# Kernel tuning notes

Hardware: AMD Instinct MI355X
Metric: run time of the kernel (lower is better)

## Reference

```python
import jax, jax.numpy as jnp
import numpy as np
from jax import lax


def _gru_layer(x, w_ih, w_hh, b_ih, b_hh):
    """PyTorch-style GRU layer (gate order r, z, n). x: [B,T,I] -> ([B,T,H], [B,H])."""
    B, T, _ = x.shape
    H = w_hh.shape[1]
    # Precompute all input-side gate projections in one big GEMM: [B,T,3H]
    xg = jnp.einsum('bti,gi->btg', x, w_ih) + b_ih

    def step(h, xg_t):
        hg = h @ w_hh.T + b_hh                      # [B,3H]
        xr, xz, xn = jnp.split(xg_t, 3, axis=-1)
        hr, hz, hn = jnp.split(hg, 3, axis=-1)
        r = jax.nn.sigmoid(xr + hr)
        z = jax.nn.sigmoid(xz + hz)
        n = jnp.tanh(xn + r * hn)
        h_new = (1.0 - z) * n + z * h
        return h_new, h_new

    h0 = jnp.zeros((B, H), dtype=x.dtype)
    h_last, hs = lax.scan(step, h0, jnp.swapaxes(xg, 0, 1))  # scan over time
    return jnp.swapaxes(hs, 0, 1), h_last


def setup_inputs() -> dict:
    key = jax.random.key(0)
    ks = jax.random.split(key, 13)
    B, T, I, H = 64, 512, 2048, 128

    def u(k, shape, fan_in):
        bound = 1.0 / np.sqrt(fan_in)
        return jax.random.uniform(k, shape, jnp.float32, -bound, bound)

    return {
        'x': jax.random.normal(ks[0], (B, T, I), jnp.float32),
        'w_ih0': u(ks[1], (3 * H, I), H),
        'w_hh0': u(ks[2], (3 * H, H), H),
        'b_ih0': u(ks[3], (3 * H,), H),
        'b_hh0': u(ks[4], (3 * H,), H),
        'w_ih1': u(ks[5], (3 * H, H), H),
        'w_hh1': u(ks[6], (3 * H, H), H),
        'b_ih1': u(ks[7], (3 * H,), H),
        'b_hh1': u(ks[8], (3 * H,), H),
        'w_fc1': u(ks[9], (64, H), H),
        'b_fc1': u(ks[10], (64,), H),
        'w_fc2': u(ks[11], (1, 64), 64),
        'b_fc2': u(ks[12], (1,), 64),
    }


def reference(x, w_ih0, w_hh0, b_ih0, b_hh0, w_ih1, w_hh1, b_ih1, b_hh1,
              w_fc1, b_fc1, w_fc2, b_fc2):
    # 2-layer GRU (inter-layer dropout is identity in eval mode)
    h1_seq, _ = _gru_layer(x, w_ih0, w_hh0, b_ih0, b_hh0)
    _, h_last = _gru_layer(h1_seq, w_ih1, w_hh1, b_ih1, b_hh1)
    # MLP head: fc1 -> ReLU -> (dropout=identity in eval) -> fc2
    y = jax.nn.relu(h_last @ w_fc1.T + b_fc1)
    return y @ w_fc2.T + b_fc2  # [B, 1]
```

## Files before the change

### kernel.cpp

```cpp
#include <hip/hip_runtime.h>
#include <cstdint>
#include <cstddef>

typedef float f32x4 __attribute__((ext_vector_type(4)));
typedef float f32x2 __attribute__((ext_vector_type(2)));
typedef short s16x8 __attribute__((ext_vector_type(8)));
typedef unsigned short u16;

static __device__ __forceinline__ u16 f2bf(float f) {
    uint32_t x = __float_as_uint(f);
    x += 0x7fffu + ((x >> 16) & 1u);
    return (u16)(x >> 16);
}
static __device__ __forceinline__ float bf2f(u16 h) {
    return __uint_as_float(((uint32_t)h) << 16);
}

static __device__ __forceinline__ void bar_lds() {
    asm volatile("s_waitcnt lgkmcnt(0)" ::: "memory");
    __builtin_amdgcn_s_barrier();
    asm volatile("" ::: "memory");
}

__global__ void k_zero(int* __restrict__ p, int n) {
    int i = blockIdx.x * 256 + threadIdx.x;
    if (i < n) p[i] = 0;
}

__global__ void k_split(const float* __restrict__ src, u16* __restrict__ hi,
                        u16* __restrict__ lo, int n) {
    int i = blockIdx.x * 256 + threadIdx.x;
    if (i < n) {
        float f = src[i];
        u16 h = f2bf(f);
        hi[i] = h;
        lo[i] = f2bf(f - bf2f(h));
    }
}

__global__ __launch_bounds__(256, 2)
void k_gemm(const float* __restrict__ A, const u16* __restrict__ Wh,
            const u16* __restrict__ Wl, const float* __restrict__ bias,
            float* __restrict__ C, int K) {
    __shared__ __align__(16) u16 sm[32768];

    const int tid  = threadIdx.x;
    const int lane = tid & 63;
    const int wave = tid >> 6;
    const int wm = wave >> 1, wn = wave & 1;

    int g = blockIdx.x;
    int xcd = g & 7, ix = g >> 3;
    int q3 = ix / 3;
    int mb = xcd + 8 * q3;
    int nb = ix - 3 * q3;
    const long m0 = (long)mb * 128;
    const int  n0 = nb * 128;

    f32x4 acc[4][4];
    const f32x4 vzero = {0.f, 0.f, 0.f, 0.f};
#pragma unroll
    for (int i = 0; i < 4; ++i)
#pragma unroll
        for (int j = 0; j < 4; ++j) acc[i][j] = vzero;

    const int ar = tid >> 1;
    const int ac = (tid & 1) * 16;
    const float* aptr = A + (m0 + ar) * (long)K + ac;
    const int br = tid >> 2;
    const int bc = (tid & 3) * 8;
    const u16* bhp = Wh + (long)(n0 + br) * K + bc;
    const u16* blp = Wl + (long)(n0 + br) * K + bc;

    const int ksteps = K >> 5;
    f32x4 a0, a1, a2, a3;

    {
        a0 = *(const f32x4*)(aptr + 0);
        a1 = *(const f32x4*)(aptr + 4);
        a2 = *(const f32x4*)(aptr + 8);
        a3 = *(const f32x4*)(aptr + 12);
#pragma unroll
        for (int c = 0; c < 2; ++c) {
            const u16* sh = bhp + (long)(c * 64) * K;
            const u16* sl = blp + (long)(c * 64) * K;
            u16* dh = &sm[8192  + c * 2048 + wave * 512];
            u16* dl = &sm[12288 + c * 2048 + wave * 512];
            __builtin_amdgcn_global_load_lds((const __attribute__((address_space(1))) void*)sh,
                                             (__attribute__((address_space(3))) void*)dh, 16, 0, 0);
            __builtin_amdgcn_global_load_lds((const __attribute__((address_space(1))) void*)sl,
                                             (__attribute__((address_space(3))) void*)dl, 16, 0, 0);
        }
        float fr[16] = {a0.x,a0.y,a0.z,a0.w, a1.x,a1.y,a1.z,a1.w,
                        a2.x,a2.y,a2.z,a2.w, a3.x,a3.y,a3.z,a3.w};
        s16x8 h0, h1, l0, l1;
#pragma unroll
        for (int i = 0; i < 8; ++i) {
            u16 hh = f2bf(fr[i]);     h0[i] = (short)hh; l0[i] = (short)f2bf(fr[i] - bf2f(hh));
            u16 hh2 = f2bf(fr[8+i]);  h1[i] = (short)hh2; l1[i] = (short)f2bf(fr[8+i] - bf2f(hh2));
        }
        u16* dh = &sm[ar * 32 + ac];
        u16* dl = &sm[4096 + ar * 32 + ac];
        *(s16x8*)dh = h0; *(s16x8*)(dh + 8) = h1;
        *(s16x8*)dl = l0; *(s16x8*)(dl + 8) = l1;
    }
    __syncthreads();

    for (int ks = 0; ks < ksteps; ++ks) {
        const int cur = ks & 1, nxt = cur ^ 1;
        const bool more = (ks + 1 < ksteps);
        if (more) {
            const int k0 = (ks + 1) << 5;
            a0 = *(const f32x4*)(aptr + k0 + 0);
            a1 = *(const f32x4*)(aptr + k0 + 4);
            a2 = *(const f32x4*)(aptr + k0 + 8);
            a3 = *(const f32x4*)(aptr + k0 + 12);
#pragma unroll
            for (int c = 0; c < 2; ++c) {
                const u16* sh = bhp + (long)(c * 64) * K + k0;
                const u16* sl = blp + (long)(c * 64) * K + k0;
                u16* dh = &sm[nxt * 16384 + 8192  + c * 2048 + wave * 512];
                u16* dl = &sm[nxt * 16384 + 12288 + c * 2048 + wave * 512];
                __builtin_amdgcn_global_load_lds((const __attribute__((address_space(1))) void*)sh,
                                                 (__attribute__((address_space(3))) void*)dh, 16, 0, 0);
                __builtin_amdgcn_global_load_lds((const __attribute__((address_space(1))) void*)sl,
                                                 (__attribute__((address_space(3))) void*)dl, 16, 0, 0);
            }
        }
        {
            const u16* base = &sm[cur * 16384];
            const int koff = (lane >> 4) * 8;
            const int rsel = lane & 15;
            s16x8 ah[4], al[4];
#pragma unroll
            for (int f = 0; f < 4; ++f) {
                int row = wm * 64 + f * 16 + rsel;
                ah[f] = *(const s16x8*)&base[row * 32 + koff];
                al[f] = *(const s16x8*)&base[4096 + row * 32 + koff];
            }
#pragma unroll
            for (int j = 0; j < 4; ++j) {
                int row = wn * 64 + j * 16 + rsel;
                s16x8 bh = *(const s16x8*)&base[8192  + row * 32 + koff];
                s16x8 bl = *(const s16x8*)&base[12288 + row * 32 + koff];
#pragma unroll
                for (int f = 0; f < 4; ++f) {
                    acc[f][j] = __builtin_amdgcn_mfma_f32_16x16x32_bf16(ah[f], bh, acc[f][j], 0, 0, 0);
                    acc[f][j] = __builtin_amdgcn_mfma_f32_16x16x32_bf16(ah[f], bl, acc[f][j], 0, 0, 0);
                    acc[f][j] = __builtin_amdgcn_mfma_f32_16x16x32_bf16(al[f], bh, acc[f][j], 0, 0, 0);
                }
            }
        }
        if (more) {
            float fr[16] = {a0.x,a0.y,a0.z,a0.w, a1.x,a1.y,a1.z,a1.w,
                            a2.x,a2.y,a2.z,a2.w, a3.x,a3.y,a3.z,a3.w};
            s16x8 h0, h1, l0, l1;
#pragma unroll
            for (int i = 0; i < 8; ++i) {
                u16 hh = f2bf(fr[i]);     h0[i] = (short)hh; l0[i] = (short)f2bf(fr[i] - bf2f(hh));
                u16 hh2 = f2bf(fr[8+i]);  h1[i] = (short)hh2; l1[i] = (short)f2bf(fr[8+i] - bf2f(hh2));
            }
            u16* dh = &sm[nxt * 16384 + ar * 32 + ac];
            u16* dl = &sm[nxt * 16384 + 4096 + ar * 32 + ac];
            *(s16x8*)dh = h0; *(s16x8*)(dh + 8) = h1;
            *(s16x8*)dl = l0; *(s16x8*)(dl + 8) = l1;
        }
        __syncthreads();
    }

    const int r0 = (lane >> 4) << 2;
    const int cn = lane & 15;
#pragma unroll
    for (int f = 0; f < 4; ++f) {
        const long mrow = m0 + wm * 64 + f * 16 + r0;
#pragma unroll
        for (int j = 0; j < 4; ++j) {
            const int n = n0 + wn * 64 + j * 16 + cn;
            const float bv = bias[n];
            float* o = C + mrow * 384 + n;
#pragma unroll
            for (int jj = 0; jj < 4; ++jj) o[(long)jj * 384] = acc[f][j][jj] + bv;
        }
    }
}


struct SmemRecur { float hsh[128]; float hp[8][384]; };
struct SmemGemm  { u16 ah[16 * 128]; u16 al[16 * 128]; };
union Smem {
    SmemRecur r;
    SmemGemm  g;
    char force_one_block_per_cu[98304];
};

#define R_ISSUE(BUF, G) do {                                                  \
    const int _G = (G);                                                       \
    if (_G < 128 && tid < 128) {                                              \
        if (!isL0 && (_G & 3) == 0) {                                         \
            if ((tid & 63) == 0) {                                            \
                while (atomicAdd(&waitflag[b * 32 + (_G >> 2)], 0) == 0)      \
                    __builtin_amdgcn_s_sleep(8);                              \
            }                                                                 \
            __threadfence();                                                  \
        }                                                                     \
        const float* _p = xgb + (size_t)(4 * _G) * 384 + tid;                 \
        BUF[0] = _p[0];    BUF[1] = _p[128];   BUF[2]  = _p[256];             \
        BUF[3] = _p[384];  BUF[4] = _p[512];   BUF[5]  = _p[640];             \
        BUF[6] = _p[768];  BUF[7] = _p[896];   BUF[8]  = _p[1024];            \
        BUF[9] = _p[1152]; BUF[10] = _p[1280]; BUF[11] = _p[1408];            \
    } } while (0)

#define R_STEP(T, BUF, J) do {                                                \
    const int _t = (T);                                                       \
    f32x4 _h0 = *(const f32x4*)(sm.hsh + 16 * w + 0);                         \
    f32x4 _h1 = *(const f32x4*)(sm.hsh + 16 * w + 4);                         \
    f32x4 _h2 = *(const f32x4*)(sm.hsh + 16 * w + 8);                         \
    f32x4 _h3 = *(const f32x4*)(sm.hsh + 16 * w + 12);                        \
    float _ha[16];                                                            \
    _ha[0]=_h0[0];  _ha[1]=_h0[1];  _ha[2]=_h0[2];  _ha[3]=_h0[3];            \
    _ha[4]=_h1[0];  _ha[5]=_h1[1];  _ha[6]=_h1[2];  _ha[7]=_h1[3];            \
    _ha[8]=_h2[0];  _ha[9]=_h2[1];  _ha[10]=_h2[2]; _ha[11]=_h2[3];           \
    _ha[12]=_h3[0]; _ha[13]=_h3[1]; _ha[14]=_h3[2]; _ha[15]=_h3[3];           \
    float _s0=0.f,_s1=0.f,_s2=0.f,_s3=0.f,_s4=0.f,_s5=0.f;                    \
    _Pragma("unroll")                                                         \
    for (int _i = 0; _i < 16; ++_i) {                                         \
        const float _hv = _ha[_i];                                            \
        _s0 = fmaf(_hv, wr[0][_i], _s0); _s1 = fmaf(_hv, wr[1][_i], _s1);     \
        _s2 = fmaf(_hv, wr[2][_i], _s2); _s3 = fmaf(_hv, wr[3][_i], _s3);     \
        _s4 = fmaf(_hv, wr[4][_i], _s4); _s5 = fmaf(_hv, wr[5][_i], _s5);     \
    }                                                                         \
    *(f32x2*)&sm.hp[w][g6 + 0] = (f32x2){_s0, _s1};                           \
    *(f32x2*)&sm.hp[w][g6 + 2] = (f32x2){_s2, _s3};                           \
    *(f32x2*)&sm.hp[w][g6 + 4] = (f32x2){_s4, _s5};                           \
    const bool _pub = isL0 && _t > 0 && (_t & 15) == 0;                       \
    if (_pub && tid < 128) asm volatile("s_waitcnt vmcnt(12)" ::: "memory");  \
    bar_lds();                                                                \
    if (_pub && tid == 0) {                                                   \
        __threadfence();                                                      \
        atomicExch(&setflag[b * 32 + ((_t >> 4) - 1)], 1);                    \
    }                                                                         \
    if (tid < 128) {                                                          \
        const int _c = tid;                                                   \
        float _hr = bhr, _hz = bhz, _hn = bhn;                                \
        _Pragma("unroll")                                                     \
        for (int _q = 0; _q < 8; ++_q) {                                      \
            _hr += sm.hp[_q][_c];                                             \
            _hz += sm.hp[_q][128 + _c];                                       \
            _hn += sm.hp[_q][256 + _c];                                       \
        }                                                                     \
        const float _xr = BUF[(J) * 3 + 0];                                   \
        const float _xz = BUF[(J) * 3 + 1];                                   \
        const float _xn = BUF[(J) * 3 + 2];                                   \
        const float _r = 1.f / (1.f + __expf(-(_xr + _hr)));                  \
        const float _z = 1.f / (1.f + __expf(-(_xz + _hz)));                  \
        float _a = _xn + _r * _hn;                                            \
        _a = fminf(fmaxf(_a, -15.f), 15.f);                                   \
        const float _e = __expf(2.f * _a);                                    \
        const float _n = (_e - 1.f) / (_e + 1.f);                             \
        hreg = (1.f - _z) * _n + _z * hreg;                                   \
        sm.hsh[_c] = hreg;                                                    \
        if (isL0) hseq[((size_t)(b * 512 + _t)) * 128 + _c] = hreg;           \
    }                                                                         \
    bar_lds();                                                                \
} while (0)

__device__ __forceinline__ void recur_role(
    bool isL0, int b, const float* __restrict__ xg,
    const float* __restrict__ whh, const float* __restrict__ bhh,
    float* __restrict__ hseq, int* __restrict__ setflag, int* __restrict__ waitflag,
    const float* __restrict__ wfc1, const float* __restrict__ bfc1,
    const float* __restrict__ wfc2, const float* __restrict__ bfc2,
    float* __restrict__ out, SmemRecur& sm)
{
    const int tid  = threadIdx.x;
    const int w    = tid >> 6;
    const int lane = tid & 63;
    const int g6   = 6 * lane;

    float wr[6][16];
#pragma unroll
    for (int j = 0; j < 6; ++j) {
        const float* p = whh + (size_t)(g6 + j) * 128 + 16 * w;
#pragma unroll
        for (int i4 = 0; i4 < 4; ++i4) {
            f32x4 v = *(const f32x4*)(p + 4 * i4);
            wr[j][4*i4+0] = v[0]; wr[j][4*i4+1] = v[1];
            wr[j][4*i4+2] = v[2]; wr[j][4*i4+3] = v[3];
        }
    }
    float bhr = 0.f, bhz = 0.f, bhn = 0.f, hreg = 0.f;
    if (tid < 128) {
        bhr = bhh[tid]; bhz = bhh[128 + tid]; bhn = bhh[256 + tid];
        sm.hsh[tid] = 0.f;
    }
    const float* xgb = xg + (size_t)b * 512 * 384;

    float pA[12], pB[12];
    R_ISSUE(pA, 0);
    R_ISSUE(pB, 1);
    __syncthreads();

    for (int gp = 0; gp < 64; ++gp) {
        const int t0 = gp * 8;
        R_STEP(t0 + 0, pA, 0); R_STEP(t0 + 1, pA, 1);
        R_STEP(t0 + 2, pA, 2); R_STEP(t0 + 3, pA, 3);
        R_ISSUE(pA, 2 * gp + 2);
        R_STEP(t0 + 4, pB, 0); R_STEP(t0 + 5, pB, 1);
        R_STEP(t0 + 6, pB, 2); R_STEP(t0 + 7, pB, 3);
        R_ISSUE(pB, 2 * gp + 3);
    }

    if (isL0) {
        if (tid < 128) asm volatile("s_waitcnt vmcnt(0)" ::: "memory");
        __syncthreads();
        if (tid == 0) { __threadfence(); atomicExch(&setflag[b * 32 + 31], 1); }
    }

    if (!isL0 && tid < 64) {
        const float* wv = wfc1 + tid * 128;
        float acc = bfc1[tid];
#pragma unroll 8
        for (int c = 0; c < 128; ++c) acc = fmaf(sm.hsh[c], wv[c], acc);
        float p = fmaxf(acc, 0.f) * wfc2[tid];
#pragma unroll
        for (int off = 32; off > 0; off >>= 1) p += __shfl_down(p, off);
        if (tid == 0) out[b] = p + bfc2[0];
    }
}

__device__ __forceinline__ void worker_role(
    int wk, const float* __restrict__ h1, float* __restrict__ xg,
    const float* __restrict__ wih1, const float* __restrict__ bih1,
    int* __restrict__ h1flag, int* __restrict__ xgflag, SmemGemm& sm)
{
    const int tid = threadIdx.x, lane = tid & 63, w = tid >> 6;
    const int rsel = lane & 15, koff = (lane >> 4) * 8;

    s16x8 bh[3][4], bl[3][4];
    float bias[3];
#pragma unroll
    for (int nfi = 0; nfi < 3; ++nfi) {
        const int n = (3 * w + nfi) * 16 + rsel;
        bias[nfi] = bih1[n];
#pragma unroll
        for (int ks = 0; ks < 4; ++ks) {
            const float* p = wih1 + n * 128 + ks * 32 + koff;
            f32x4 v0 = *(const f32x4*)p, v1 = *(const f32x4*)(p + 4);
            float fv[8] = {v0[0],v0[1],v0[2],v0[3], v1[0],v1[1],v1[2],v1[3]};
            s16x8 hh, ll;
#pragma unroll
            for (int i = 0; i < 8; ++i) {
                u16 h = f2bf(fv[i]); hh[i] = (short)h; ll[i] = (short)f2bf(fv[i] - bf2f(h));
            }
            bh[nfi][ks] = hh; bl[nfi][ks] = ll;
        }
    }

    for (int j = wk; j < 2048; j += 128) {
        const int c = j >> 6, b = j & 63;
        if (tid == 0) {
            while (atomicAdd(&h1flag[b * 32 + c], 0) == 0) __builtin_amdgcn_s_sleep(8);
            __threadfence();
        }
        __syncthreads();
        if (tid < 256) {
            const int r = tid >> 4, c0 = (tid & 15) * 8;
            const float* p = h1 + ((size_t)(b * 512 + c * 16 + r)) * 128 + c0;
            f32x4 v0 = *(const f32x4*)p, v1 = *(const f32x4*)(p + 4);
            float fv[8] = {v0[0],v0[1],v0[2],v0[3], v1[0],v1[1],v1[2],v1[3]};
            s16x8 hh, ll;
#pragma unroll
            for (int i = 0; i < 8; ++i) {
                u16 h = f2bf(fv[i]); hh[i] = (short)h; ll[i] = (short)f2bf(fv[i] - bf2f(h));
            }
            const int sc = c0 ^ ((r & 7) << 3);
            *(s16x8*)&sm.ah[r * 128 + sc] = hh;
            *(s16x8*)&sm.al[r * 128 + sc] = ll;
        }
        __syncthreads();

        f32x4 acc[3];
        const f32x4 vz = {0.f, 0.f, 0.f, 0.f};
        acc[0] = vz; acc[1] = vz; acc[2] = vz;
#pragma unroll
        for (int ks = 0; ks < 4; ++ks) {
            const int si = rsel * 128 + ((ks * 32 + koff) ^ ((rsel & 7) << 3));
            s16x8 a_h = *(const s16x8*)&sm.ah[si];
            s16x8 a_l = *(const s16x8*)&sm.al[si];
#pragma unroll
            for (int nfi = 0; nfi < 3; ++nfi) {
                acc[nfi] = __builtin_amdgcn_mfma_f32_16x16x32_bf16(a_h, bh[nfi][ks], acc[nfi], 0, 0, 0);
                acc[nfi] = __builtin_amdgcn_mfma_f32_16x16x32_bf16(a_h, bl[nfi][ks], acc[nfi], 0, 0, 0);
                acc[nfi] = __builtin_amdgcn_mfma_f32_16x16x32_bf16(a_l, bh[nfi][ks], acc[nfi], 0, 0, 0);
            }
        }
#pragma unroll
        for (int nfi = 0; nfi < 3; ++nfi) {
            const int n = (3 * w + nfi) * 16 + rsel;
#pragma unroll
            for (int jj = 0; jj < 4; ++jj) {
                const int m = (lane >> 4) * 4 + jj;
                xg[((size_t)(b * 512 + c * 16 + m)) * 384 + n] = acc[nfi][jj] + bias[nfi];
            }
        }
        __syncthreads();
        if (tid == 0) {
            __threadfence();
            atomicExch(&xgflag[b * 32 + c], 1);
        }
    }
}

__global__ __launch_bounds__(512, 2)
void k_fused(float* __restrict__ xg, float* __restrict__ h1,
             const float* __restrict__ whh0, const float* __restrict__ bhh0,
             const float* __restrict__ wih1, const float* __restrict__ bih1,
             const float* __restrict__ whh1, const float* __restrict__ bhh1,
             const float* __restrict__ wfc1, const float* __restrict__ bfc1,
             const float* __restrict__ wfc2, const float* __restrict__ bfc2,
             float* __restrict__ out, int* __restrict__ h1flag, int* __restrict__ xgflag)
{
    __shared__ __align__(16) Smem sm;
    const int bid = blockIdx.x;
    if (bid < 64) {
        recur_role(true, bid, xg, whh0, bhh0, h1, h1flag, nullptr,
                   nullptr, nullptr, nullptr, nullptr, nullptr, sm.r);
    } else if (bid < 128) {
        recur_role(false, bid - 64, xg, whh1, bhh1, nullptr, nullptr, xgflag,
                   wfc1, bfc1, wfc2, bfc2, out, sm.r);
    } else {
        worker_role(bid - 128, h1, xg, wih1, bih1, h1flag, xgflag, sm.g);
    }
}

extern "C" void kernel_launch(void* const* d_in, const int* in_sizes, int n_in,
                              void* d_out, int out_size, void* d_ws, size_t ws_size,
                              hipStream_t stream) {
    const float* x     = (const float*)d_in[0];
    const float* w_ih0 = (const float*)d_in[1];
    const float* w_hh0 = (const float*)d_in[2];
    const float* b_ih0 = (const float*)d_in[3];
    const float* b_hh0 = (const float*)d_in[4];
    const float* w_ih1 = (const float*)d_in[5];
    const float* w_hh1 = (const float*)d_in[6];
    const float* b_ih1 = (const float*)d_in[7];
    const float* b_hh1 = (const float*)d_in[8];
    const float* w_fc1 = (const float*)d_in[9];
    const float* b_fc1 = (const float*)d_in[10];
    const float* w_fc2 = (const float*)d_in[11];
    const float* b_fc2 = (const float*)d_in[12];
    float* out = (float*)d_out;
    (void)in_sizes; (void)n_in; (void)out_size; (void)ws_size;

    char* ws = (char*)d_ws;
    float* xg     = (float*)(ws + 0);
    float* h1     = (float*)(ws + 50331648);
    u16*   w0h    = (u16*)(ws + 67108864);
    u16*   w0l    = (u16*)(ws + 68681728);
    int*   h1flag = (int*)(ws + 70254592);
    int*   xgflag = h1flag + 2048;

    k_zero<<<16, 256, 0, stream>>>(h1flag, 4096);
    k_split<<<3072, 256, 0, stream>>>(w_ih0, w0h, w0l, 384 * 2048);
    k_gemm<<<768, 256, 0, stream>>>(x, w0h, w0l, b_ih0, xg, 2048);
    k_fused<<<256, 512, 0, stream>>>(xg, h1, w_hh0, b_hh0, w_ih1, b_ih1,
                                     w_hh1, b_hh1, w_fc1, b_fc1, w_fc2, b_fc2,
                                     out, h1flag, xgflag);
}
```

Measured before the change: 621.9 us.

## Batch 16 sequences per recurrent block using split-bf16 MFMA for hidden GEMM

Each recurrent block now handles 16 batch rows instead of one, so only 8 blocks run the GRU recurrences. The h @ W_hh product moves from scalar FMAs with an LDS partial-sum reduction to 3-term split-bf16 MFMA, with h double-buffered as bf16 hi/lo fragments in LDS, which removes one barrier per step. Worker blocks grow to 248, signal with per-group counters, and the launch bound is relaxed to one block per CU. The aim is to shorten the serial per-timestep critical path, at the cost of split-bf16 precision error and coarser synchronisation.

```diff
diff --git a/kernel.cpp b/kernel.cpp
--- a/kernel.cpp
+++ b/kernel.cpp
@@ -3,7 +3,6 @@
 #include <cstddef>
 
 typedef float f32x4 __attribute__((ext_vector_type(4)));
-typedef float f32x2 __attribute__((ext_vector_type(2)));
 typedef short s16x8 __attribute__((ext_vector_type(8)));
 typedef unsigned short u16;
 
@@ -185,153 +184,176 @@
 }
 
 
-struct SmemRecur { float hsh[128]; float hp[8][384]; };
-struct SmemGemm  { u16 ah[16 * 128]; u16 al[16 * 128]; };
+struct SmemRecur {
+    u16 frag[2][2][2048];
+    float h2buf[16][128];
+};
+struct SmemGemm  { u16 ah[2048]; u16 al[2048]; };
 union Smem {
     SmemRecur r;
     SmemGemm  g;
     char force_one_block_per_cu[98304];
 };
 
-#define R_ISSUE(BUF, G) do {                                                  \
-    const int _G = (G);                                                       \
-    if (_G < 128 && tid < 128) {                                              \
-        if (!isL0 && (_G & 3) == 0) {                                         \
-            if ((tid & 63) == 0) {                                            \
-                while (atomicAdd(&waitflag[b * 32 + (_G >> 2)], 0) == 0)      \
+#define PF(R_, Z_, N_, T_) do {                                               \
+    const int _pt = (T_);                                                     \
+    if (_pt < 512) {                                                          \
+        if (!isL0 && (_pt & 15) == 0) {                                       \
+            if (lane == 0) {                                                  \
+                while (atomicAdd(&waitcnt[g * 32 + (_pt >> 4)], 0) < 16)      \
                     __builtin_amdgcn_s_sleep(8);                              \
             }                                                                 \
             __threadfence();                                                  \
         }                                                                     \
-        const float* _p = xgb + (size_t)(4 * _G) * 384 + tid;                 \
-        BUF[0] = _p[0];    BUF[1] = _p[128];   BUF[2]  = _p[256];             \
-        BUF[3] = _p[384];  BUF[4] = _p[512];   BUF[5]  = _p[640];             \
-        BUF[6] = _p[768];  BUF[7] = _p[896];   BUF[8]  = _p[1024];            \
-        BUF[9] = _p[1152]; BUF[10] = _p[1280]; BUF[11] = _p[1408];            \
+        const size_t _o = (size_t)_pt * 384;                                  \
+        R_[0] = bp0[_o]; Z_[0] = bp0[_o + 128]; N_[0] = bp0[_o + 256];        \
+        R_[1] = bp1[_o]; Z_[1] = bp1[_o + 128]; N_[1] = bp1[_o + 256];        \
+        R_[2] = bp2[_o]; Z_[2] = bp2[_o + 128]; N_[2] = bp2[_o + 256];        \
+        R_[3] = bp3[_o]; Z_[3] = bp3[_o + 128]; N_[3] = bp3[_o + 256];        \
     } } while (0)
 
-#define R_STEP(T, BUF, J) do {                                                \
-    const int _t = (T);                                                       \
-    f32x4 _h0 = *(const f32x4*)(sm.hsh + 16 * w + 0);                         \
-    f32x4 _h1 = *(const f32x4*)(sm.hsh + 16 * w + 4);                         \
-    f32x4 _h2 = *(const f32x4*)(sm.hsh + 16 * w + 8);                         \
-    f32x4 _h3 = *(const f32x4*)(sm.hsh + 16 * w + 12);                        \
-    float _ha[16];                                                            \
-    _ha[0]=_h0[0];  _ha[1]=_h0[1];  _ha[2]=_h0[2];  _ha[3]=_h0[3];            \
-    _ha[4]=_h1[0];  _ha[5]=_h1[1];  _ha[6]=_h1[2];  _ha[7]=_h1[3];            \
-    _ha[8]=_h2[0];  _ha[9]=_h2[1];  _ha[10]=_h2[2]; _ha[11]=_h2[3];           \
-    _ha[12]=_h3[0]; _ha[13]=_h3[1]; _ha[14]=_h3[2]; _ha[15]=_h3[3];           \
-    float _s0=0.f,_s1=0.f,_s2=0.f,_s3=0.f,_s4=0.f,_s5=0.f;                    \
-    _Pragma("unroll")                                                         \
-    for (int _i = 0; _i < 16; ++_i) {                                         \
-        const float _hv = _ha[_i];                                            \
-        _s0 = fmaf(_hv, wr[0][_i], _s0); _s1 = fmaf(_hv, wr[1][_i], _s1);     \
-        _s2 = fmaf(_hv, wr[2][_i], _s2); _s3 = fmaf(_hv, wr[3][_i], _s3);     \
-        _s4 = fmaf(_hv, wr[4][_i], _s4); _s5 = fmaf(_hv, wr[5][_i], _s5);     \
+#define RSTEP(T_, R_, Z_, N_) do {                                            \
+    const int _t = (T_);                                                      \
+    f32x4 accr = {R_[0] + bhr, R_[1] + bhr, R_[2] + bhr, R_[3] + bhr};        \
+    f32x4 accz = {Z_[0] + bhz, Z_[1] + bhz, Z_[2] + bhz, Z_[3] + bhz};        \
+    f32x4 accn = {bhn, bhn, bhn, bhn};                                        \
+    const float _xn0 = N_[0], _xn1 = N_[1], _xn2 = N_[2], _xn3 = N_[3];       \
+    {                                                                         \
+        const u16* _hb = &sm.frag[p][0][0];                                   \
+        const u16* _lb = &sm.frag[p][1][0];                                   \
+        _Pragma("unroll")                                                     \
+        for (int kk = 0; kk < 4; ++kk) {                                      \
+            const int _fo = (kk * 4 + qk) * 128 + col * 8;                    \
+            s16x8 _ah = *(const s16x8*)&_hb[_fo];                             \
+            s16x8 _al = *(const s16x8*)&_lb[_fo];                             \
+            accr = __builtin_amdgcn_mfma_f32_16x16x32_bf16(_ah, wbh[0][kk], accr, 0, 0, 0); \
+            accz = __builtin_amdgcn_mfma_f32_16x16x32_bf16(_ah, wbh[1][kk], accz, 0, 0, 0); \
+            accn = __builtin_amdgcn_mfma_f32_16x16x32_bf16(_ah, wbh[2][kk], accn, 0, 0, 0); \
+            accr = __builtin_amdgcn_mfma_f32_16x16x32_bf16(_ah, wbl[0][kk], accr, 0, 0, 0); \
+            accz = __builtin_amdgcn_mfma_f32_16x16x32_bf16(_ah, wbl[1][kk], accz, 0, 0, 0); \
+            accn = __builtin_amdgcn_mfma_f32_16x16x32_bf16(_ah, wbl[2][kk], accn, 0, 0, 0); \
+            accr = __builtin_amdgcn_mfma_f32_16x16x32_bf16(_al, wbh[0][kk], accr, 0, 0, 0); \
+            accz = __builtin_amdgcn_mfma_f32_16x16x32_bf16(_al, wbh[1][kk], accz, 0, 0, 0); \
+            accn = __builtin_amdgcn_mfma_f32_16x16x32_bf16(_al, wbh[2][kk], accn, 0, 0, 0); \
+        }                                                                     \
     }                                                                         \
-    *(f32x2*)&sm.hp[w][g6 + 0] = (f32x2){_s0, _s1};                           \
-    *(f32x2*)&sm.hp[w][g6 + 2] = (f32x2){_s2, _s3};                           \
-    *(f32x2*)&sm.hp[w][g6 + 4] = (f32x2){_s4, _s5};                           \
-    const bool _pub = isL0 && _t > 0 && (_t & 15) == 0;                       \
-    if (_pub && tid < 128) asm volatile("s_waitcnt vmcnt(12)" ::: "memory");  \
+    {                                                                         \
+        u16* _wh = &sm.frag[p ^ 1][0][0];                                     \
+        u16* _wl = &sm.frag[p ^ 1][1][0];                                     \
+        const float _xna[4] = {_xn0, _xn1, _xn2, _xn3};                       \
+        _Pragma("unroll")                                                     \
+        for (int j = 0; j < 4; ++j) {                                         \
+            const float _r = 1.f / (1.f + __expf(-accr[j]));                  \
+            const float _z = 1.f / (1.f + __expf(-accz[j]));                  \
+            float _a = _xna[j] + _r * accn[j];                                \
+            _a = fminf(fmaxf(_a, -15.f), 15.f);                               \
+            const float _e = __expf(2.f * _a);                                \
+            const float _n = (_e - 1.f) / (_e + 1.f);                         \
+            const float _h = (1.f - _z) * _n + _z * hold[j];                  \
+            hold[j] = _h;                                                     \
+            const u16 _hh = f2bf(_h);                                         \
+            _wh[fa + j * 8] = _hh;                                            \
+            _wl[fa + j * 8] = f2bf(_h - bf2f(_hh));                           \
+            if (isL0) hseq[hb0 + (size_t)j * 65536 + (size_t)_t * 128] = _h;  \
+        }                                                                     \
+    }                                                                         \
+    PF(R_, Z_, N_, _t + 2);                                                   \
+    const bool _pub = isL0 && ((_t & 15) == 15) && (_t < 511);                \
+    if (_pub) asm volatile("s_waitcnt vmcnt(12)" ::: "memory");               \
     bar_lds();                                                                \
     if (_pub && tid == 0) {                                                   \
         __threadfence();                                                      \
-        atomicExch(&setflag[b * 32 + ((_t >> 4) - 1)], 1);                    \
+        atomicExch(&setflag[g * 32 + (_t >> 4)], 1);                          \
     }                                                                         \
-    if (tid < 128) {                                                          \
-        const int _c = tid;                                                   \
-        float _hr = bhr, _hz = bhz, _hn = bhn;                                \
-        _Pragma("unroll")                                                     \
-        for (int _q = 0; _q < 8; ++_q) {                                      \
-            _hr += sm.hp[_q][_c];                                             \
-            _hz += sm.hp[_q][128 + _c];                                       \
-            _hn += sm.hp[_q][256 + _c];                                       \
-        }                                                                     \
-        const float _xr = BUF[(J) * 3 + 0];                                   \
-        const float _xz = BUF[(J) * 3 + 1];                                   \
-        const float _xn = BUF[(J) * 3 + 2];                                   \
-        const float _r = 1.f / (1.f + __expf(-(_xr + _hr)));                  \
-        const float _z = 1.f / (1.f + __expf(-(_xz + _hz)));                  \
-        float _a = _xn + _r * _hn;                                            \
-        _a = fminf(fmaxf(_a, -15.f), 15.f);                                   \
-        const float _e = __expf(2.f * _a);                                    \
-        const float _n = (_e - 1.f) / (_e + 1.f);                             \
-        hreg = (1.f - _z) * _n + _z * hreg;                                   \
-        sm.hsh[_c] = hreg;                                                    \
-        if (isL0) hseq[((size_t)(b * 512 + _t)) * 128 + _c] = hreg;           \
-    }                                                                         \
-    bar_lds();                                                                \
+    p ^= 1;                                                                   \
 } while (0)
 
 __device__ __forceinline__ void recur_role(
-    bool isL0, int b, const float* __restrict__ xg,
+    bool isL0, int g, const float* __restrict__ xg,
     const float* __restrict__ whh, const float* __restrict__ bhh,
-    float* __restrict__ hseq, int* __restrict__ setflag, int* __restrict__ waitflag,
+    float* __restrict__ hseq, int* __restrict__ setflag, int* __restrict__ waitcnt,
     const float* __restrict__ wfc1, const float* __restrict__ bfc1,
     const float* __restrict__ wfc2, const float* __restrict__ bfc2,
     float* __restrict__ out, SmemRecur& sm)
 {
-    const int tid  = threadIdx.x;
-    const int w    = tid >> 6;
-    const int lane = tid & 63;
-    const int g6   = 6 * lane;
-
-    float wr[6][16];
-#pragma unroll
-    for (int j = 0; j < 6; ++j) {
-        const float* p = whh + (size_t)(g6 + j) * 128 + 16 * w;
-#pragma unroll
-        for (int i4 = 0; i4 < 4; ++i4) {
-            f32x4 v = *(const f32x4*)(p + 4 * i4);
-            wr[j][4*i4+0] = v[0]; wr[j][4*i4+1] = v[1];
-            wr[j][4*i4+2] = v[2]; wr[j][4*i4+3] = v[3];
-        }
-    }
-    float bhr = 0.f, bhz = 0.f, bhn = 0.f, hreg = 0.f;
-    if (tid < 128) {
-        bhr = bhh[tid]; bhz = bhh[128 + tid]; bhn = bhh[256 + tid];
-        sm.hsh[tid] = 0.f;
-    }
-    const float* xgb = xg + (size_t)b * 512 * 384;
-
-    float pA[12], pB[12];
-    R_ISSUE(pA, 0);
-    R_ISSUE(pB, 1);
+    const int tid = threadIdx.x, lane = tid & 63, w = tid >> 6;
+    const int col = lane & 15;
+    const int qk  = lane >> 4;
+    const int gr  = 16 * w + col;
+
+    s16x8 wbh[3][4], wbl[3][4];
+#pragma unroll
+    for (int gs = 0; gs < 3; ++gs)
+#pragma unroll
+        for (int kk = 0; kk < 4; ++kk) {
+            const float* p = whh + (size_t)(gs * 128 + gr) * 128 + kk * 32 + qk * 8;
+            f32x4 v0 = *(const f32x4*)p, v1 = *(const f32x4*)(p + 4);
+            float fv[8] = {v0[0], v0[1], v0[2], v0[3], v1[0], v1[1], v1[2], v1[3]};
+            s16x8 hh, ll;
+#pragma unroll
+            for (int i = 0; i < 8; ++i) {
+                u16 h = f2bf(fv[i]); hh[i] = (short)h; ll[i] = (short)f2bf(fv[i] - bf2f(h));
+            }
+            wbh[gs][kk] = hh; wbl[gs][kk] = ll;
+        }
+    const float bhr = bhh[gr], bhz = bhh[128 + gr], bhn = bhh[256 + gr];
+    f32x4 hold = {0.f, 0.f, 0.f, 0.f};
+
+    const size_t bstr = (size_t)512 * 384;
+    const float* bp0 = xg + (size_t)(16 * g + qk * 4 + 0) * bstr + gr;
+    const float* bp1 = xg + (size_t)(16 * g + qk * 4 + 1) * bstr + gr;
+    const float* bp2 = xg + (size_t)(16 * g + qk * 4 + 2) * bstr + gr;
+    const float* bp3 = xg + (size_t)(16 * g + qk * 4 + 3) * bstr + gr;
+    const size_t hb0 = ((size_t)(16 * g) + qk * 4) * 65536 + gr;
+    const int fa = ((gr >> 3) * 128) + (qk * 32) + (gr & 7);
+
+    {
+        uint32_t* z32 = (uint32_t*)&sm.frag[0][0][0];
+#pragma unroll
+        for (int i = 0; i < 4; ++i) z32[tid + 512 * i] = 0;
+    }
+    f32x4 rA, zA, nA, rB, zB, nB;
+    PF(rA, zA, nA, 0);
+    PF(rB, zB, nB, 1);
     __syncthreads();
 
-    for (int gp = 0; gp < 64; ++gp) {
-        const int t0 = gp * 8;
-        R_STEP(t0 + 0, pA, 0); R_STEP(t0 + 1, pA, 1);
-        R_STEP(t0 + 2, pA, 2); R_STEP(t0 + 3, pA, 3);
-        R_ISSUE(pA, 2 * gp + 2);
-        R_STEP(t0 + 4, pB, 0); R_STEP(t0 + 5, pB, 1);
-        R_STEP(t0 + 6, pB, 2); R_STEP(t0 + 7, pB, 3);
-        R_ISSUE(pB, 2 * gp + 3);
+    int p = 0;
+    for (int i = 0; i < 256; ++i) {
+        RSTEP(2 * i,     rA, zA, nA);
+        RSTEP(2 * i + 1, rB, zB, nB);
     }
 
     if (isL0) {
-        if (tid < 128) asm volatile("s_waitcnt vmcnt(0)" ::: "memory");
-        __syncthreads();
-        if (tid == 0) { __threadfence(); atomicExch(&setflag[b * 32 + 31], 1); }
-    }
-
-    if (!isL0 && tid < 64) {
-        const float* wv = wfc1 + tid * 128;
-        float acc = bfc1[tid];
-#pragma unroll 8
-        for (int c = 0; c < 128; ++c) acc = fmaf(sm.hsh[c], wv[c], acc);
-        float p = fmaxf(acc, 0.f) * wfc2[tid];
-#pragma unroll
-        for (int off = 32; off > 0; off >>= 1) p += __shfl_down(p, off);
-        if (tid == 0) out[b] = p + bfc2[0];
+        asm volatile("s_waitcnt vmcnt(0)" ::: "memory");
+        __syncthreads();
+        if (tid == 0) { __threadfence(); atomicExch(&setflag[g * 32 + 31], 1); }
+    }
+
+    if (!isL0) {
+#pragma unroll
+        for (int j = 0; j < 4; ++j) sm.h2buf[qk * 4 + j][gr] = hold[j];
+        __syncthreads();
+        const int hb_ = tid >> 5, l_ = tid & 31;
+        const float* hv = sm.h2buf[hb_];
+        const float* w0 = wfc1 + l_ * 128;
+        const float* w1 = wfc1 + (l_ + 32) * 128;
+        float d0 = bfc1[l_], d1 = bfc1[l_ + 32];
+#pragma unroll 4
+        for (int c2 = 0; c2 < 128; ++c2) {
+            d0 = fmaf(hv[c2], w0[c2], d0);
+            d1 = fmaf(hv[c2], w1[c2], d1);
+        }
+        float pv = fmaxf(d0, 0.f) * wfc2[l_] + fmaxf(d1, 0.f) * wfc2[l_ + 32];
+#pragma unroll
+        for (int off = 16; off > 0; off >>= 1) pv += __shfl_down(pv, off, 32);
+        if (l_ == 0) out[16 * g + hb_] = pv + bfc2[0];
     }
 }
 
 __device__ __forceinline__ void worker_role(
     int wk, const float* __restrict__ h1, float* __restrict__ xg,
     const float* __restrict__ wih1, const float* __restrict__ bih1,
-    int* __restrict__ h1flag, int* __restrict__ xgflag, SmemGemm& sm)
+    int* __restrict__ h1flag, int* __restrict__ xgcnt, SmemGemm& sm)
 {
     const int tid = threadIdx.x, lane = tid & 63, w = tid >> 6;
     const int rsel = lane & 15, koff = (lane >> 4) * 8;
@@ -346,7 +368,7 @@
         for (int ks = 0; ks < 4; ++ks) {
             const float* p = wih1 + n * 128 + ks * 32 + koff;
             f32x4 v0 = *(const f32x4*)p, v1 = *(const f32x4*)(p + 4);
-            float fv[8] = {v0[0],v0[1],v0[2],v0[3], v1[0],v1[1],v1[2],v1[3]};
+            float fv[8] = {v0[0], v0[1], v0[2], v0[3], v1[0], v1[1], v1[2], v1[3]};
             s16x8 hh, ll;
 #pragma unroll
             for (int i = 0; i < 8; ++i) {
@@ -356,10 +378,11 @@
         }
     }
 
-    for (int j = wk; j < 2048; j += 128) {
+    for (int j = wk; j < 2048; j += 248) {
         const int c = j >> 6, b = j & 63;
         if (tid == 0) {
-            while (atomicAdd(&h1flag[b * 32 + c], 0) == 0) __builtin_amdgcn_s_sleep(8);
+            while (atomicAdd(&h1flag[(b >> 4) * 32 + c], 0) == 0)
+                __builtin_amdgcn_s_sleep(8);
             __threadfence();
         }
         __syncthreads();
@@ -367,7 +390,7 @@
             const int r = tid >> 4, c0 = (tid & 15) * 8;
             const float* p = h1 + ((size_t)(b * 512 + c * 16 + r)) * 128 + c0;
             f32x4 v0 = *(const f32x4*)p, v1 = *(const f32x4*)(p + 4);
-            float fv[8] = {v0[0],v0[1],v0[2],v0[3], v1[0],v1[1],v1[2],v1[3]};
+            float fv[8] = {v0[0], v0[1], v0[2], v0[3], v1[0], v1[1], v1[2], v1[3]};
             s16x8 hh, ll;
 #pragma unroll
             for (int i = 0; i < 8; ++i) {
@@ -406,30 +429,30 @@
         __syncthreads();
         if (tid == 0) {
             __threadfence();
-            atomicExch(&xgflag[b * 32 + c], 1);
-        }
-    }
-}
-
-__global__ __launch_bounds__(512, 2)
+            atomicAdd(&xgcnt[(b >> 4) * 32 + c], 1);
+        }
+    }
+}
+
+__global__ __launch_bounds__(512, 1)
 void k_fused(float* __restrict__ xg, float* __restrict__ h1,
              const float* __restrict__ whh0, const float* __restrict__ bhh0,
              const float* __restrict__ wih1, const float* __restrict__ bih1,
              const float* __restrict__ whh1, const float* __restrict__ bhh1,
              const float* __restrict__ wfc1, const float* __restrict__ bfc1,
              const float* __restrict__ wfc2, const float* __restrict__ bfc2,
-             float* __restrict__ out, int* __restrict__ h1flag, int* __restrict__ xgflag)
+             float* __restrict__ out, int* __restrict__ h1flag, int* __restrict__ xgcnt)
 {
     __shared__ __align__(16) Smem sm;
     const int bid = blockIdx.x;
-    if (bid < 64) {
+    if (bid < 4) {
         recur_role(true, bid, xg, whh0, bhh0, h1, h1flag, nullptr,
                    nullptr, nullptr, nullptr, nullptr, nullptr, sm.r);
-    } else if (bid < 128) {
-        recur_role(false, bid - 64, xg, whh1, bhh1, nullptr, nullptr, xgflag,
+    } else if (bid < 8) {
+        recur_role(false, bid - 4, xg, whh1, bhh1, nullptr, nullptr, xgcnt,
                    wfc1, bfc1, wfc2, bfc2, out, sm.r);
     } else {
-        worker_role(bid - 128, h1, xg, wih1, bih1, h1flag, xgflag, sm.g);
+        worker_role(bid - 8, h1, xg, wih1, bih1, h1flag, xgcnt, sm.g);
     }
 }
 
@@ -458,12 +481,12 @@
     u16*   w0h    = (u16*)(ws + 67108864);
     u16*   w0l    = (u16*)(ws + 68681728);
     int*   h1flag = (int*)(ws + 70254592);
-    int*   xgflag = h1flag + 2048;
-
-    k_zero<<<16, 256, 0, stream>>>(h1flag, 4096);
+    int*   xgcnt  = h1flag + 128;
+
+    k_zero<<<1, 256, 0, stream>>>(h1flag, 256);
     k_split<<<3072, 256, 0, stream>>>(w_ih0, w0h, w0l, 384 * 2048);
     k_gemm<<<768, 256, 0, stream>>>(x, w0h, w0l, b_ih0, xg, 2048);
     k_fused<<<256, 512, 0, stream>>>(xg, h1, w_hh0, b_hh0, w_ih1, b_ih1,
                                      w_hh1, b_hh1, w_fc1, b_fc1, w_fc2, b_fc2,
-                                     out, h1flag, xgflag);
-}
+                                     out, h1flag, xgcnt);
+}
```

After: 1.083 ms. 74.2% more time.
